# Kernel tuning notes

Measured on AMD Instinct MI355X. Metric: run time of the kernel, lower is better.

## Reference

```python
import jax, jax.numpy as jnp
import numpy as np

N, E, G = 50000, 800000, 1000
F, FM, L, H, T = 128, 16, 7, 128, 12
DIN, DH = 2 * F + 1, 2 * (2 * F + 1)  # 257, 514
UIN, UH = F + FM, 2 * F               # 144, 256

def swish(x):
    return x * jax.nn.sigmoid(x)

def setup_inputs() -> dict:
    key = jax.random.key(0)
    ks = jax.random.split(key, 16)
    pos = jax.random.normal(ks[0], (N, 3), dtype=jnp.float32)
    zi = jax.random.randint(ks[1], (N,), 0, 5)
    z = jnp.array([1, 6, 7, 8, 9], dtype=jnp.int64)[zi]  # valid atomic numbers
    edge_index = jax.random.randint(ks[2], (2, E), 0, N)
    batch = jnp.sort(jax.random.randint(ks[3], (N,), 0, G))
    def w(k, shape, fan_in):
        return jax.random.normal(k, shape, dtype=jnp.float32) / np.sqrt(fan_in)
    return {
        'pos': pos, 'z': z, 'edge_index': edge_index, 'batch': batch,
        'emb': jax.random.normal(ks[4], (5, F), dtype=jnp.float32),
        'W_msg1': w(ks[5], (L, DIN, DH), DIN), 'b_msg1': jnp.zeros((L, DH), jnp.float32),
        'W_msg2': w(ks[6], (L, DH, FM), DH), 'b_msg2': jnp.zeros((L, FM), jnp.float32),
        'W_up1': w(ks[7], (L, UIN, UH), UIN), 'b_up1': jnp.zeros((L, UH), jnp.float32),
        'W_up2': w(ks[8], (L, UH, F), UH), 'b_up2': jnp.zeros((L, F), jnp.float32),
        'Wp1': w(ks[9], (F, H), F), 'bp1': jnp.zeros((H,), jnp.float32),
        'Wp2': w(ks[10], (H, H), H), 'bp2': jnp.zeros((H,), jnp.float32),
        'Wr1': w(ks[11], (H, H), H), 'br1': jnp.zeros((H,), jnp.float32),
        'Wr2': w(ks[12], (H, T), H), 'br2': jnp.zeros((T,), jnp.float32),
        'n_graphs': G,
    }

def reference(pos, z, edge_index, batch, emb, W_msg1, b_msg1, W_msg2, b_msg2,
              W_up1, b_up1, W_up2, b_up2, Wp1, bp1, Wp2, bp2, Wr1, br1, Wr2, br2,
              n_graphs):
    n = pos.shape[0]
    atomic = jnp.array([-1, 0, -1, -1, -1, -1, 1, 2, 3, 4])
    h = emb[atomic[z]]                                  # [N, F]
    src, dst = edge_index[0], edge_index[1]
    d = pos[src] - pos[dst]
    norm2 = jnp.sum(d * d, axis=1)                      # [E] squared distance
    for l in range(W_msg1.shape[0]):
        inp = jnp.concatenate([h[dst], h[src], norm2[:, None]], axis=1)  # x_i, x_j, norm2
        m = swish(inp @ W_msg1[l] + b_msg1[l])
        m = swish(m @ W_msg2[l] + b_msg2[l])            # [E, FM]
        agg = jax.ops.segment_sum(m, dst, num_segments=n)  # aggregate at target nodes
        u = jnp.concatenate([agg, h], axis=1)           # [N, F+FM]
        u = swish(u @ W_up1[l] + b_up1[l])
        h = u @ W_up2[l] + b_up2[l] + h                 # residual update
    proj = swish(h @ Wp1 + bp1) @ Wp2 + bp2             # node_proj
    pooled = jax.ops.segment_sum(proj, batch, num_segments=n_graphs)  # global_add_pool
    return swish(pooled @ Wr1 + br1) @ Wr2 + br2        # readout [G, T]
```

## Files before the change

kernel.cpp:

```cpp
#include <hip/hip_runtime.h>
#include <hip/hip_bf16.h>
#include <cstdint>
#include <cstddef>

typedef _Float16 h16x8 __attribute__((ext_vector_type(8)));
typedef float f32x4 __attribute__((ext_vector_type(4)));

#define NSTRIPE 2

__device__ __forceinline__ void splitf16(float v, _Float16& hi, _Float16& lo) {
    hi = (_Float16)v;
    lo = (_Float16)(v - (float)hi);
}
__device__ __forceinline__ float swish_fast(float x) {
    float e = __expf(-x);
    return x * __builtin_amdgcn_rcpf(1.0f + e);
}

__global__ void init_nodes(const int* __restrict__ z, const float* __restrict__ emb,
                           float* __restrict__ hf, _Float16* __restrict__ hhi,
                           _Float16* __restrict__ hlo, int N) {
    int tid = blockIdx.x * 256 + threadIdx.x;
    int n = tid >> 7, f = tid & 127;
    int zv = z[n];
    int idx5 = (zv == 1) ? 0 : (zv - 5);
    float v = emb[idx5 * 128 + f];
    hf[tid] = v;
    _Float16 hi, lo;
    splitf16(v, hi, lo);
    hhi[tid] = hi;
    hlo[tid] = lo;
}

__device__ __forceinline__ int edge_key(int d, int s, int N, int stripeSz) {
    return (d / stripeSz) * N + s;
}

__global__ void hist_kernel(const int* __restrict__ src, const int* __restrict__ dst,
                            int* __restrict__ hist, int E, int N, int stripeSz) {
    int e = blockIdx.x * 256 + threadIdx.x;
    if (e < E) atomicAdd(&hist[edge_key(dst[e], src[e], N, stripeSz)], 1);
}

__global__ void scan_p1(const int* __restrict__ hist, int* __restrict__ blocksum, int KN) {
    __shared__ int s[256];
    int idx = blockIdx.x * 256 + threadIdx.x;
    int v = (idx < KN) ? hist[idx] : 0;
    s[threadIdx.x] = v;
    __syncthreads();
    for (int d = 128; d > 0; d >>= 1) {
        if (threadIdx.x < d) s[threadIdx.x] += s[threadIdx.x + d];
        __syncthreads();
    }
    if (threadIdx.x == 0) blocksum[blockIdx.x] = s[0];
}

__global__ void scan_p2(int* __restrict__ blocksum, int NB) {
    __shared__ int s[1024];
    int t = threadIdx.x;
    int v = (t < NB) ? blocksum[t] : 0;
    s[t] = v;
    __syncthreads();
    for (int d = 1; d < 1024; d <<= 1) {
        int x = (t >= d) ? s[t - d] : 0;
        __syncthreads();
        s[t] += x;
        __syncthreads();
    }
    if (t < NB) blocksum[t] = s[t] - v;
}

__global__ void scan_p3(const int* __restrict__ hist, const int* __restrict__ blocksum,
                        int* __restrict__ cursor, int KN) {
    __shared__ int s[256];
    int idx = blockIdx.x * 256 + threadIdx.x;
    int v = (idx < KN) ? hist[idx] : 0;
    s[threadIdx.x] = v;
    __syncthreads();
    for (int d = 1; d < 256; d <<= 1) {
        int x = (threadIdx.x >= d) ? s[threadIdx.x - d] : 0;
        __syncthreads();
        s[threadIdx.x] += x;
        __syncthreads();
    }
    if (idx < KN) cursor[idx] = blocksum[blockIdx.x] + s[threadIdx.x] - v;
}

__global__ void scatter_kernel(const int* __restrict__ src, const int* __restrict__ dst,
                               int* __restrict__ cursor, int* __restrict__ perm,
                               int E, int N, int stripeSz) {
    int e = blockIdx.x * 256 + threadIdx.x;
    if (e < E) {
        int p = atomicAdd(&cursor[edge_key(dst[e], src[e], N, stripeSz)], 1);
        perm[p] = e;
    }
}

__global__ void reorder_kernel(const int* __restrict__ perm, const int* __restrict__ src,
                               const int* __restrict__ dst, const float* __restrict__ pos,
                               int* __restrict__ srcS, int* __restrict__ dstS,
                               float* __restrict__ n2S, int E) {
    int i = blockIdx.x * 256 + threadIdx.x;
    if (i >= E) return;
    int e = perm[i];
    int si = src[e], di = dst[e];
    srcS[i] = si;
    dstS[i] = di;
    float dx = pos[si * 3 + 0] - pos[di * 3 + 0];
    float dy = pos[si * 3 + 1] - pos[di * 3 + 1];
    float dz = pos[si * 3 + 2] - pos[di * 3 + 2];
    n2S[i] = dx * dx + dy * dy + dz * dz;
}

__global__ void pack_msg1(const float* __restrict__ Wm1, const float* __restrict__ bm1,
                          const float* __restrict__ Wm2,
                          _Float16* __restrict__ Bp1A, float* __restrict__ biasA,
                          _Float16* __restrict__ w1cA, _Float16* __restrict__ W2pA) {
    int l = blockIdx.y;
    const float* Wm1l = Wm1 + (size_t)l * 257 * 514;
    const float* bm1l = bm1 + (size_t)l * 514;
    const float* Wm2l = Wm2 + (size_t)l * 514 * 16;
    _Float16* Bp1 = Bp1A + (size_t)l * 139264;
    float* bias1088 = biasA + (size_t)l * 1088;
    _Float16* w1c = w1cA + (size_t)l * 544;
    _Float16* W2p = W2pA + (size_t)l * 8704;

    int t = blockIdx.x * 256 + threadIdx.x;
    int i = t & 7;
    int lane = (t >> 3) & 63;
    int rest = t >> 9;
    int cb = rest % 68;
    int ks = rest / 68;
    int k = ks * 32 + ((lane >> 4) << 3) + i;
    int ch = cb * 16 + (lane & 15);
    float val;
    if (ch < 544) {
        val = (ch < 514) ? Wm1l[k * 514 + ch] : 0.f;
    } else {
        int c = ch - 544;
        val = (c < 514) ? Wm1l[(128 + k) * 514 + c] : 0.f;
    }
    Bp1[t] = (_Float16)val;
    if (t < 1088) bias1088[t] = (t < 514) ? bm1l[t] : 0.f;
    if (t < 544) w1c[t] = (_Float16)((t < 514) ? Wm1l[256 * 514 + t] : 0.f);
    if (t < 8704) {
        int i2 = t & 7, lane2 = (t >> 3) & 63, ks2 = t >> 9;
        int k2 = ks2 * 32 + ((lane2 >> 4) << 3) + i2;
        int c2 = lane2 & 15;
        W2p[t] = (_Float16)((k2 < 514) ? Wm2l[k2 * 16 + c2] : 0.f);
    }
}

__global__ void pack_generic(const float* __restrict__ Wall, size_t strideW, int K, int Nc,
                             _Float16* __restrict__ BpAll, size_t strideB) {
    int l = blockIdx.y;
    const float* W = Wall + (size_t)l * strideW;
    _Float16* Bp = BpAll + (size_t)l * strideB;
    int t = blockIdx.x * 256 + threadIdx.x;
    int i = t & 7;
    int lane = (t >> 3) & 63;
    int rest = t >> 9;
    int CB = Nc >> 4;
    int cb = rest % CB;
    int ks = rest / CB;
    int k = ks * 32 + ((lane >> 4) << 3) + i;
    int c = cb * 16 + (lane & 15);
    float val = (k < K) ? W[(size_t)k * Nc + c] : 0.f;
    Bp[t] = (_Float16)val;
}

__global__ __launch_bounds__(256) void tab_gemm(
    const _Float16* __restrict__ Ahi, const _Float16* __restrict__ Alo,
    const _Float16* __restrict__ Bp, const float* __restrict__ bias,
    _Float16* __restrict__ TA, _Float16* __restrict__ TB, float* __restrict__ agg, int N) {
    {
        int base = blockIdx.x * 1024 + threadIdx.x;
#pragma unroll
        for (int q = 0; q < 4; ++q) {
            int idx = base + q * 256;
            if (idx < N * 16) agg[idx] = 0.f;
        }
    }
    int lane = threadIdx.x & 63;
    int wid = threadIdx.x >> 6;
    int row0 = blockIdx.x * 64 + wid * 16;
    if (row0 >= N) return;
    const size_t arow = (size_t)(row0 + (lane & 15)) * 128;
    const int ak = (lane >> 4) * 8;
    h16x8 ah[4], al[4];
#pragma unroll
    for (int ks = 0; ks < 4; ++ks) {
        ah[ks] = *(const h16x8*)(Ahi + arow + ks * 32 + ak);
        al[ks] = *(const h16x8*)(Alo + arow + ks * 32 + ak);
    }
    int col16 = lane & 15;
    int rb = (lane >> 4) * 4;
    for (int cb = 0; cb < 68; ++cb) {
        f32x4 acc = {0.f, 0.f, 0.f, 0.f};
#pragma unroll
        for (int ks = 0; ks < 4; ++ks) {
            h16x8 bh = *(const h16x8*)(Bp + ((size_t)(ks * 68 + cb) * 64 + lane) * 8);
            acc = __builtin_amdgcn_mfma_f32_16x16x32_f16(ah[ks], bh, acc, 0, 0, 0);
            acc = __builtin_amdgcn_mfma_f32_16x16x32_f16(al[ks], bh, acc, 0, 0, 0);
        }
        int col = cb * 16 + col16;
        float bv = bias[col];
        if (cb < 34) {
#pragma unroll
            for (int i = 0; i < 4; ++i)
                TA[(size_t)(row0 + rb + i) * 544 + col] = (_Float16)(acc[i] + bv);
        } else {
#pragma unroll
            for (int i = 0; i < 4; ++i)
                TB[(size_t)(row0 + rb + i) * 544 + (col - 544)] = (_Float16)(acc[i] + bv);
        }
    }
}

template <int KS, int CB, int MODE>
__global__ __launch_bounds__(256) void gemmA(
    const _Float16* __restrict__ Ahi, const _Float16* __restrict__ Alo, int lda,
    const _Float16* __restrict__ Bp, const float* __restrict__ bias,
    _Float16* __restrict__ outB, _Float16* __restrict__ outB2, int ldoB,
    float* __restrict__ outF, int ldoF, const float* __restrict__ resid,
    const int* __restrict__ batch, float* __restrict__ pooled, int N) {
    int lane = threadIdx.x & 63;
    int wid = threadIdx.x >> 6;
    int row0 = blockIdx.x * 64 + wid * 16;
    if (row0 >= N) return;
    const size_t arow = (size_t)(row0 + (lane & 15)) * lda;
    const int ak = (lane >> 4) * 8;
    h16x8 ah[KS], al[KS];
#pragma unroll
    for (int ks = 0; ks < KS; ++ks) {
        ah[ks] = *(const h16x8*)(Ahi + arow + ks * 32 + ak);
        al[ks] = *(const h16x8*)(Alo + arow + ks * 32 + ak);
    }
    int col16 = lane & 15;
    int rb = (lane >> 4) * 4;
    for (int cb = 0; cb < CB; ++cb) {
        f32x4 acc = {0.f, 0.f, 0.f, 0.f};
#pragma unroll
        for (int ks = 0; ks < KS; ++ks) {
            h16x8 bh = *(const h16x8*)(Bp + ((size_t)(ks * CB + cb) * 64 + lane) * 8);
            acc = __builtin_amdgcn_mfma_f32_16x16x32_f16(ah[ks], bh, acc, 0, 0, 0);
            acc = __builtin_amdgcn_mfma_f32_16x16x32_f16(al[ks], bh, acc, 0, 0, 0);
        }
        int col = cb * 16 + col16;
        float bv = bias[col];
#pragma unroll
        for (int i = 0; i < 4; ++i) {
            int row = row0 + rb + i;
            float v = acc[i] + bv;
            if (MODE == 1) {
                float s = swish_fast(v);
                _Float16 hi, lo;
                splitf16(s, hi, lo);
                outB[(size_t)row * ldoB + col] = hi;
                outB2[(size_t)row * ldoB + col] = lo;
            } else if (MODE == 2) {
                float h = v + resid[(size_t)row * ldoF + col];
                outF[(size_t)row * ldoF + col] = h;
                _Float16 hi, lo;
                splitf16(h, hi, lo);
                outB[(size_t)row * ldoB + col] = hi;
                outB2[(size_t)row * ldoB + col] = lo;
            } else {
                unsafeAtomicAdd(&pooled[(size_t)batch[row] * 128 + col], v);
            }
        }
    }
}

__global__ __launch_bounds__(256) void up1_gemm(
    const float* __restrict__ agg, const float* __restrict__ hf,
    const _Float16* __restrict__ Bp, const float* __restrict__ bias,
    _Float16* __restrict__ uhi, _Float16* __restrict__ ulo, int N) {
    int lane = threadIdx.x & 63;
    int wid = threadIdx.x >> 6;
    int row0 = blockIdx.x * 64 + wid * 16;
    if (row0 >= N) return;
    int r = row0 + (lane & 15);
    const int ak = (lane >> 4) * 8;
    h16x8 ah[5], al[5];
#pragma unroll
    for (int ks = 0; ks < 5; ++ks) {
        int c0 = ks * 32 + ak;
        f32x4 v0, v1;
        if (c0 < 16) {
            v0 = *(const f32x4*)(agg + (size_t)r * 16 + c0);
            v1 = *(const f32x4*)(agg + (size_t)r * 16 + c0 + 4);
        } else if (c0 < 144) {
            v0 = *(const f32x4*)(hf + (size_t)r * 128 + c0 - 16);
            v1 = *(const f32x4*)(hf + (size_t)r * 128 + c0 - 12);
        } else {
            v0 = f32x4{0.f, 0.f, 0.f, 0.f};
            v1 = f32x4{0.f, 0.f, 0.f, 0.f};
        }
        h16x8 hi8, lo8;
#pragma unroll
        for (int jj = 0; jj < 8; ++jj) {
            float x = (jj < 4) ? v0[jj] : v1[jj - 4];
            _Float16 h, l;
            splitf16(x, h, l);
            hi8[jj] = h;
            lo8[jj] = l;
        }
        ah[ks] = hi8;
        al[ks] = lo8;
    }
    int col16 = lane & 15;
    int rb = (lane >> 4) * 4;
    for (int cb = 0; cb < 16; ++cb) {
        f32x4 acc = {0.f, 0.f, 0.f, 0.f};
#pragma unroll
        for (int ks = 0; ks < 5; ++ks) {
            h16x8 bh = *(const h16x8*)(Bp + ((size_t)(ks * 16 + cb) * 64 + lane) * 8);
            acc = __builtin_amdgcn_mfma_f32_16x16x32_f16(ah[ks], bh, acc, 0, 0, 0);
            acc = __builtin_amdgcn_mfma_f32_16x16x32_f16(al[ks], bh, acc, 0, 0, 0);
        }
        int col = cb * 16 + col16;
        float bv = bias[col];
#pragma unroll
        for (int i = 0; i < 4; ++i) {
            int row = row0 + rb + i;
            float s = swish_fast(acc[i] + bv);
            _Float16 hi, lo;
            splitf16(s, hi, lo);
            uhi[(size_t)row * 256 + col] = hi;
            ulo[(size_t)row * 256 + col] = lo;
        }
    }
}

__global__ __launch_bounds__(256) void edge_kernel(
    const _Float16* __restrict__ TA, const _Float16* __restrict__ TB,
    const _Float16* __restrict__ w1c, const _Float16* __restrict__ W2p,
    const float* __restrict__ bm2l,
    const int* __restrict__ srcS, const int* __restrict__ dstS,
    const float* __restrict__ n2S, float* __restrict__ agg) {
    __shared__ _Float16 sW[8704];
    __shared__ _Float16 sw1[544];
    for (int t = threadIdx.x; t < 1088; t += 256)
        ((h16x8*)sW)[t] = ((const h16x8*)W2p)[t];
    for (int t = threadIdx.x; t < 544; t += 256) sw1[t] = w1c[t];
    __syncthreads();

    int lane = threadIdx.x & 63;
    int wid = threadIdx.x >> 6;
    int ebase = blockIdx.x * 128 + wid * 32;
    int rr = lane & 15;
    int e0 = ebase + rr;
    int e1 = ebase + 16 + rr;
    int di0 = dstS[e0], si0 = srcS[e0];
    int di1 = dstS[e1], si1 = srcS[e1];
    _Float16 n20 = (_Float16)n2S[e0];
    _Float16 n21 = (_Float16)n2S[e1];
    const int ak = (lane >> 4) * 8;
    const _Float16* pa0 = TA + (size_t)di0 * 544 + ak;
    const _Float16* pb0 = TB + (size_t)si0 * 544 + ak;
    const _Float16* pa1 = TA + (size_t)di1 * 544 + ak;
    const _Float16* pb1 = TB + (size_t)si1 * 544 + ak;

    const _Float16 nl2e = (_Float16)(-1.44269504f);
    f32x4 acc0 = {0.f, 0.f, 0.f, 0.f};
    f32x4 acc1 = {0.f, 0.f, 0.f, 0.f};

    h16x8 bufA[16], bufB[16], bufT[4];

    auto issue4 = [&](h16x8* buf, int K) {
#pragma unroll
        for (int q = 0; q < 4; ++q) {
            buf[q * 4 + 0] = *(const h16x8*)(pa0 + (K + q) * 32);
            buf[q * 4 + 1] = *(const h16x8*)(pb0 + (K + q) * 32);
            buf[q * 4 + 2] = *(const h16x8*)(pa1 + (K + q) * 32);
            buf[q * 4 + 3] = *(const h16x8*)(pb1 + (K + q) * 32);
        }
    };
    auto step = [&](const h16x8* buf, int q, int ks) {
        h16x8 va0 = buf[q * 4 + 0], vb0 = buf[q * 4 + 1];
        h16x8 va1 = buf[q * 4 + 2], vb1 = buf[q * 4 + 3];
        h16x8 wv = *(const h16x8*)(sw1 + ks * 32 + ak);
        h16x8 x0 = va0 + vb0 + wv * n20;
        h16x8 ev0 = __builtin_elementwise_exp2(x0 * nl2e);
        h16x8 d0 = ev0 + (_Float16)1.0f;
        h16x8 r0;
#pragma unroll
        for (int j = 0; j < 8; ++j) r0[j] = __builtin_amdgcn_rcph(d0[j]);
        h16x8 m0 = x0 * r0;
        h16x8 x1 = va1 + vb1 + wv * n21;
        h16x8 ev1 = __builtin_elementwise_exp2(x1 * nl2e);
        h16x8 d1 = ev1 + (_Float16)1.0f;
        h16x8 r1;
#pragma unroll
        for (int j = 0; j < 8; ++j) r1[j] = __builtin_amdgcn_rcph(d1[j]);
        h16x8 m1 = x1 * r1;
        h16x8 bh = *(const h16x8*)(sW + (ks * 64 + lane) * 8);
        acc0 = __builtin_amdgcn_mfma_f32_16x16x32_f16(m0, bh, acc0, 0, 0, 0);
        acc1 = __builtin_amdgcn_mfma_f32_16x16x32_f16(m1, bh, acc1, 0, 0, 0);
    };

    issue4(bufA, 0);
    __builtin_amdgcn_sched_barrier(0);
    issue4(bufB, 4);
    __builtin_amdgcn_sched_barrier(0);
#pragma unroll
    for (int q = 0; q < 4; ++q) step(bufA, q, q);
    issue4(bufA, 8);
    __builtin_amdgcn_sched_barrier(0);
#pragma unroll
    for (int q = 0; q < 4; ++q) step(bufB, q, 4 + q);
    issue4(bufB, 12);
    __builtin_amdgcn_sched_barrier(0);
#pragma unroll
    for (int q = 0; q < 4; ++q) step(bufA, q, 8 + q);
    bufT[0] = *(const h16x8*)(pa0 + 16 * 32);
    bufT[1] = *(const h16x8*)(pb0 + 16 * 32);
    bufT[2] = *(const h16x8*)(pa1 + 16 * 32);
    bufT[3] = *(const h16x8*)(pb1 + 16 * 32);
    __builtin_amdgcn_sched_barrier(0);
#pragma unroll
    for (int q = 0; q < 4; ++q) step(bufB, q, 12 + q);
    step(bufT, 0, 16);

    int col = lane & 15;
    float b2 = bm2l[col];
#pragma unroll
    for (int i = 0; i < 4; ++i) {
        int ea = ebase + (lane >> 4) * 4 + i;
        float v0 = swish_fast(acc0[i] + b2);
        unsafeAtomicAdd(&agg[(size_t)dstS[ea] * 16 + col], v0);
        int eb = ea + 16;
        float v1 = swish_fast(acc1[i] + b2);
        unsafeAtomicAdd(&agg[(size_t)dstS[eb] * 16 + col], v1);
    }
}

__global__ void readout(const float* __restrict__ pooled, const float* __restrict__ Wr1,
                        const float* __restrict__ br1, const float* __restrict__ Wr2,
                        const float* __restrict__ br2, float* __restrict__ out) {
    __shared__ float row[128];
    __shared__ float tt[128];
    int g = blockIdx.x;
    int t = threadIdx.x;
    row[t] = pooled[g * 128 + t];
    __syncthreads();
    float s = br1[t];
    for (int k = 0; k < 128; ++k) s += row[k] * Wr1[k * 128 + t];
    tt[t] = swish_fast(s);
    __syncthreads();
    if (t < 12) {
        float o = br2[t];
        for (int j = 0; j < 128; ++j) o += tt[j] * Wr2[j * 12 + t];
        out[g * 12 + t] = o;
    }
}

extern "C" void kernel_launch(void* const* d_in, const int* in_sizes, int n_in,
                              void* d_out, int out_size, void* d_ws, size_t ws_size,
                              hipStream_t stream) {
    const float* pos = (const float*)d_in[0];
    const int* z = (const int*)d_in[1];
    const int* ei = (const int*)d_in[2];
    const int* batch = (const int*)d_in[3];
    const float* emb = (const float*)d_in[4];
    const float* Wm1 = (const float*)d_in[5];
    const float* bm1 = (const float*)d_in[6];
    const float* Wm2 = (const float*)d_in[7];
    const float* bm2 = (const float*)d_in[8];
    const float* Wu1 = (const float*)d_in[9];
    const float* bu1 = (const float*)d_in[10];
    const float* Wu2 = (const float*)d_in[11];
    const float* bu2 = (const float*)d_in[12];
    const float* Wp1 = (const float*)d_in[13];
    const float* bp1v = (const float*)d_in[14];
    const float* Wp2 = (const float*)d_in[15];
    const float* bp2v = (const float*)d_in[16];
    const float* Wr1 = (const float*)d_in[17];
    const float* br1 = (const float*)d_in[18];
    const float* Wr2 = (const float*)d_in[19];
    const float* br2 = (const float*)d_in[20];

    const int N = in_sizes[0] / 3;
    const int E = in_sizes[2] / 2;
    const int G = out_size / 12;
    const int* src = ei;
    const int* dstp = ei + E;
    const int stripeSz = (N + NSTRIPE - 1) / NSTRIPE;
    const int KN = NSTRIPE * N;
    const int NB = (KN + 255) / 256;

    char* ws = (char*)d_ws;
    size_t off = 0;
    auto alloc = [&](size_t bytes) -> char* {
        char* p = ws + off;
        off += (bytes + 255) & ~(size_t)255;
        return p;
    };
    _Float16* TA = (_Float16*)alloc((size_t)N * 544 * 2);
    _Float16* TB = (_Float16*)alloc((size_t)N * 544 * 2);
    float* hf = (float*)alloc((size_t)N * 128 * 4);
    _Float16* hhi = (_Float16*)alloc((size_t)N * 128 * 2);
    _Float16* hlo = (_Float16*)alloc((size_t)N * 128 * 2);
    float* agg = (float*)alloc((size_t)N * 16 * 4);
    float* pooled = (float*)alloc((size_t)G * 128 * 4);
    int* hist = (int*)alloc((size_t)KN * 4);
    int* cursor = (int*)alloc((size_t)KN * 4);
    int* blocksum = (int*)alloc((size_t)NB * 4);
    int* perm = (int*)alloc((size_t)E * 4);
    int* srcS = (int*)alloc((size_t)E * 4);
    int* dstS = (int*)alloc((size_t)E * 4);
    float* n2S = (float*)alloc((size_t)E * 4);
    _Float16* Bp1A = (_Float16*)alloc((size_t)7 * 139264 * 2);
    float* biasA = (float*)alloc((size_t)7 * 1088 * 4);
    _Float16* w1cA = (_Float16*)alloc((size_t)7 * 544 * 2);
    _Float16* W2pA = (_Float16*)alloc((size_t)7 * 8704 * 2);
    _Float16* BpU1A = (_Float16*)alloc((size_t)7 * 40960 * 2);
    _Float16* BpU2A = (_Float16*)alloc((size_t)7 * 32768 * 2);
    _Float16* BpP1 = (_Float16*)alloc(16384 * 2);
    _Float16* BpP2 = (_Float16*)alloc(16384 * 2);

    _Float16* uhi = TA;
    _Float16* ulo = TA + (size_t)N * 256;
    _Float16* t1hi = TB;
    _Float16* t1lo = TB + (size_t)N * 128;

    init_nodes<<<(N * 128) / 256, 256, 0, stream>>>(z, emb, hf, hhi, hlo, N);

    hipMemsetAsync(hist, 0, (size_t)KN * 4, stream);
    hist_kernel<<<(E + 255) / 256, 256, 0, stream>>>(src, dstp, hist, E, N, stripeSz);
    scan_p1<<<NB, 256, 0, stream>>>(hist, blocksum, KN);
    scan_p2<<<1, 1024, 0, stream>>>(blocksum, NB);
    scan_p3<<<NB, 256, 0, stream>>>(hist, blocksum, cursor, KN);
    scatter_kernel<<<(E + 255) / 256, 256, 0, stream>>>(src, dstp, cursor, perm, E, N, stripeSz);
    reorder_kernel<<<(E + 255) / 256, 256, 0, stream>>>(perm, src, dstp, pos, srcS, dstS, n2S, E);

    pack_msg1<<<dim3(139264 / 256, 7), 256, 0, stream>>>(Wm1, bm1, Wm2, Bp1A, biasA, w1cA, W2pA);
    pack_generic<<<dim3(160, 7), 256, 0, stream>>>(Wu1, (size_t)144 * 256, 144, 256, BpU1A, 40960);
    pack_generic<<<dim3(128, 7), 256, 0, stream>>>(Wu2, (size_t)256 * 128, 256, 128, BpU2A, 32768);
    pack_generic<<<dim3(64, 1), 256, 0, stream>>>(Wp1, 0, 128, 128, BpP1, 0);
    pack_generic<<<dim3(64, 1), 256, 0, stream>>>(Wp2, 0, 128, 128, BpP2, 0);

    const int gA = (N + 63) / 64;
    for (int l = 0; l < 7; ++l) {
        tab_gemm<<<gA, 256, 0, stream>>>(hhi, hlo, Bp1A + (size_t)l * 139264,
                                         biasA + (size_t)l * 1088, TA, TB, agg, N);
        edge_kernel<<<E / 128, 256, 0, stream>>>(TA, TB, w1cA + (size_t)l * 544,
                                                 W2pA + (size_t)l * 8704, bm2 + l * 16,
                                                 srcS, dstS, n2S, agg);
        up1_gemm<<<gA, 256, 0, stream>>>(agg, hf, BpU1A + (size_t)l * 40960,
                                         bu1 + l * 256, uhi, ulo, N);
        gemmA<8, 8, 2><<<gA, 256, 0, stream>>>(
            uhi, ulo, 256, BpU2A + (size_t)l * 32768, bu2 + l * 128,
            hhi, hlo, 128, hf, 128, hf, nullptr, nullptr, N);
    }

    gemmA<4, 8, 1><<<gA, 256, 0, stream>>>(
        hhi, hlo, 128, BpP1, bp1v,
        t1hi, t1lo, 128, nullptr, 0, nullptr, nullptr, nullptr, N);
    hipMemsetAsync(pooled, 0, (size_t)G * 128 * 4, stream);
    gemmA<4, 8, 3><<<gA, 256, 0, stream>>>(
        t1hi, t1lo, 128, BpP2, bp2v,
        nullptr, nullptr, 0, nullptr, 0, nullptr, batch, pooled, N);
    readout<<<G, 128, 0, stream>>>(pooled, Wr1, br1, Wr2, br2, (float*)d_out);
}
```

Measured before the change: 2.179 ms.

## Fuse update MLP GEMMs via LDS and drop low-half split in table GEMM

The two update-MLP GEMMs are merged into one kernel. The swish(u) hi/lo tile is staged in shared memory instead of being written to global memory and reread, which removes a large intermediate round trip and a launch per layer. Separately, the per-node message table GEMM now uses only the fp16 high part of h, halving its MFMA work. The cost is extra LDS use per block (possible occupancy loss) and reduced precision in the message-table inputs.

```diff
diff --git a/kernel.cpp b/kernel.cpp
--- a/kernel.cpp
+++ b/kernel.cpp
@@ -170,7 +170,7 @@
 }
 
 __global__ __launch_bounds__(256) void tab_gemm(
-    const _Float16* __restrict__ Ahi, const _Float16* __restrict__ Alo,
+    const _Float16* __restrict__ Ahi,
     const _Float16* __restrict__ Bp, const float* __restrict__ bias,
     _Float16* __restrict__ TA, _Float16* __restrict__ TB, float* __restrict__ agg, int N) {
     {
@@ -187,12 +187,10 @@
     if (row0 >= N) return;
     const size_t arow = (size_t)(row0 + (lane & 15)) * 128;
     const int ak = (lane >> 4) * 8;
-    h16x8 ah[4], al[4];
-#pragma unroll
-    for (int ks = 0; ks < 4; ++ks) {
+    h16x8 ah[4];
+#pragma unroll
+    for (int ks = 0; ks < 4; ++ks)
         ah[ks] = *(const h16x8*)(Ahi + arow + ks * 32 + ak);
-        al[ks] = *(const h16x8*)(Alo + arow + ks * 32 + ak);
-    }
     int col16 = lane & 15;
     int rb = (lane >> 4) * 4;
     for (int cb = 0; cb < 68; ++cb) {
@@ -201,7 +199,6 @@
         for (int ks = 0; ks < 4; ++ks) {
             h16x8 bh = *(const h16x8*)(Bp + ((size_t)(ks * 68 + cb) * 64 + lane) * 8);
             acc = __builtin_amdgcn_mfma_f32_16x16x32_f16(ah[ks], bh, acc, 0, 0, 0);
-            acc = __builtin_amdgcn_mfma_f32_16x16x32_f16(al[ks], bh, acc, 0, 0, 0);
         }
         int col = cb * 16 + col16;
         float bv = bias[col];
@@ -222,7 +219,6 @@
     const _Float16* __restrict__ Ahi, const _Float16* __restrict__ Alo, int lda,
     const _Float16* __restrict__ Bp, const float* __restrict__ bias,
     _Float16* __restrict__ outB, _Float16* __restrict__ outB2, int ldoB,
-    float* __restrict__ outF, int ldoF, const float* __restrict__ resid,
     const int* __restrict__ batch, float* __restrict__ pooled, int N) {
     int lane = threadIdx.x & 63;
     int wid = threadIdx.x >> 6;
@@ -258,13 +254,6 @@
                 splitf16(s, hi, lo);
                 outB[(size_t)row * ldoB + col] = hi;
                 outB2[(size_t)row * ldoB + col] = lo;
-            } else if (MODE == 2) {
-                float h = v + resid[(size_t)row * ldoF + col];
-                outF[(size_t)row * ldoF + col] = h;
-                _Float16 hi, lo;
-                splitf16(h, hi, lo);
-                outB[(size_t)row * ldoB + col] = hi;
-                outB2[(size_t)row * ldoB + col] = lo;
             } else {
                 unsafeAtomicAdd(&pooled[(size_t)batch[row] * 128 + col], v);
             }
@@ -272,10 +261,13 @@
     }
 }
 
-__global__ __launch_bounds__(256) void up1_gemm(
-    const float* __restrict__ agg, const float* __restrict__ hf,
-    const _Float16* __restrict__ Bp, const float* __restrict__ bias,
-    _Float16* __restrict__ uhi, _Float16* __restrict__ ulo, int N) {
+__global__ __launch_bounds__(256) void up_fused(
+    const float* __restrict__ agg, const _Float16* __restrict__ Bp1,
+    const float* __restrict__ b1, const _Float16* __restrict__ Bp2,
+    const float* __restrict__ b2,
+    float* __restrict__ hf, _Float16* __restrict__ hhi, _Float16* __restrict__ hlo, int N) {
+    __shared__ _Float16 sUh[4][16][264];
+    __shared__ _Float16 sUl[4][16][264];
     int lane = threadIdx.x & 63;
     int wid = threadIdx.x >> 6;
     int row0 = blockIdx.x * 64 + wid * 16;
@@ -315,20 +307,47 @@
         f32x4 acc = {0.f, 0.f, 0.f, 0.f};
 #pragma unroll
         for (int ks = 0; ks < 5; ++ks) {
-            h16x8 bh = *(const h16x8*)(Bp + ((size_t)(ks * 16 + cb) * 64 + lane) * 8);
+            h16x8 bh = *(const h16x8*)(Bp1 + ((size_t)(ks * 16 + cb) * 64 + lane) * 8);
             acc = __builtin_amdgcn_mfma_f32_16x16x32_f16(ah[ks], bh, acc, 0, 0, 0);
             acc = __builtin_amdgcn_mfma_f32_16x16x32_f16(al[ks], bh, acc, 0, 0, 0);
         }
         int col = cb * 16 + col16;
-        float bv = bias[col];
+        float bv = b1[col];
 #pragma unroll
         for (int i = 0; i < 4; ++i) {
-            int row = row0 + rb + i;
             float s = swish_fast(acc[i] + bv);
             _Float16 hi, lo;
             splitf16(s, hi, lo);
-            uhi[(size_t)row * 256 + col] = hi;
-            ulo[(size_t)row * 256 + col] = lo;
+            sUh[wid][rb + i][col] = hi;
+            sUl[wid][rb + i][col] = lo;
+        }
+    }
+    __syncthreads();
+    h16x8 ah2[8], al2[8];
+#pragma unroll
+    for (int ks = 0; ks < 8; ++ks) {
+        ah2[ks] = *(const h16x8*)(&sUh[wid][lane & 15][ks * 32 + ak]);
+        al2[ks] = *(const h16x8*)(&sUl[wid][lane & 15][ks * 32 + ak]);
+    }
+    for (int cb = 0; cb < 8; ++cb) {
+        f32x4 acc = {0.f, 0.f, 0.f, 0.f};
+#pragma unroll
+        for (int ks = 0; ks < 8; ++ks) {
+            h16x8 bh = *(const h16x8*)(Bp2 + ((size_t)(ks * 8 + cb) * 64 + lane) * 8);
+            acc = __builtin_amdgcn_mfma_f32_16x16x32_f16(ah2[ks], bh, acc, 0, 0, 0);
+            acc = __builtin_amdgcn_mfma_f32_16x16x32_f16(al2[ks], bh, acc, 0, 0, 0);
+        }
+        int col = cb * 16 + col16;
+        float bv = b2[col];
+#pragma unroll
+        for (int i = 0; i < 4; ++i) {
+            int row = row0 + rb + i;
+            float h = acc[i] + bv + hf[(size_t)row * 128 + col];
+            hf[(size_t)row * 128 + col] = h;
+            _Float16 hi, lo;
+            splitf16(h, hi, lo);
+            hhi[(size_t)row * 128 + col] = hi;
+            hlo[(size_t)row * 128 + col] = lo;
         }
     }
 }
@@ -520,8 +539,6 @@
     _Float16* BpP1 = (_Float16*)alloc(16384 * 2);
     _Float16* BpP2 = (_Float16*)alloc(16384 * 2);
 
-    _Float16* uhi = TA;
-    _Float16* ulo = TA + (size_t)N * 256;
     _Float16* t1hi = TB;
     _Float16* t1lo = TB + (size_t)N * 128;
 
@@ -543,24 +560,22 @@
 
     const int gA = (N + 63) / 64;
     for (int l = 0; l < 7; ++l) {
-        tab_gemm<<<gA, 256, 0, stream>>>(hhi, hlo, Bp1A + (size_t)l * 139264,
+        tab_gemm<<<gA, 256, 0, stream>>>(hhi, Bp1A + (size_t)l * 139264,
                                          biasA + (size_t)l * 1088, TA, TB, agg, N);
         edge_kernel<<<E / 128, 256, 0, stream>>>(TA, TB, w1cA + (size_t)l * 544,
                                                  W2pA + (size_t)l * 8704, bm2 + l * 16,
                                                  srcS, dstS, n2S, agg);
-        up1_gemm<<<gA, 256, 0, stream>>>(agg, hf, BpU1A + (size_t)l * 40960,
-                                         bu1 + l * 256, uhi, ulo, N);
-        gemmA<8, 8, 2><<<gA, 256, 0, stream>>>(
-            uhi, ulo, 256, BpU2A + (size_t)l * 32768, bu2 + l * 128,
-            hhi, hlo, 128, hf, 128, hf, nullptr, nullptr, N);
+        up_fused<<<gA, 256, 0, stream>>>(agg, BpU1A + (size_t)l * 40960, bu1 + l * 256,
+                                         BpU2A + (size_t)l * 32768, bu2 + l * 128,
+                                         hf, hhi, hlo, N);
     }
 
     gemmA<4, 8, 1><<<gA, 256, 0, stream>>>(
         hhi, hlo, 128, BpP1, bp1v,
-        t1hi, t1lo, 128, nullptr, 0, nullptr, nullptr, nullptr, N);
+        t1hi, t1lo, 128, nullptr, nullptr, N);
     hipMemsetAsync(pooled, 0, (size_t)G * 128 * 4, stream);
     gemmA<4, 8, 3><<<gA, 256, 0, stream>>>(
         t1hi, t1lo, 128, BpP2, bp2v,
-        nullptr, nullptr, 0, nullptr, 0, nullptr, batch, pooled, N);
+        nullptr, nullptr, 0, batch, pooled, N);
     readout<<<G, 128, 0, stream>>>(pooled, Wr1, br1, Wr2, br2, (float*)d_out);
 }
```

Result: faster. 2.054 ms (-5.7%).
